# Optimization experiments

Hardware: AMD Instinct MI355X
Metric: run time of the kernel (lower is better)

Reference implementation:

```python
import jax, jax.numpy as jnp
import numpy as np

N = 100_000   # nodes
E = 1_600_000 # edges (avg degree 16)
IN = 128
OUT = 128
EPS = 1e-5    # torch BatchNorm1d default eps


def setup_inputs() -> dict:
    key = jax.random.key(0)
    k0, k1, k2 = jax.random.split(key, 3)
    x = jax.random.normal(k0, (N, IN), dtype=jnp.float32)
    edge_index = jax.random.randint(k1, (2, E), 0, N, dtype=jnp.int32)
    W = jax.random.normal(k2, (IN, OUT), dtype=jnp.float32) * (1.0 / np.sqrt(IN))
    b = jnp.zeros((OUT,), dtype=jnp.float32)
    gamma = jnp.ones((OUT,), dtype=jnp.float32)
    beta = jnp.zeros((OUT,), dtype=jnp.float32)
    return {"x": x, "edge_index": edge_index, "W": W, "b": b, "gamma": gamma, "beta": beta}


def reference(x, edge_index, W, b, gamma, beta):
    n = x.shape[0]
    # --- GCNConv: add self loops + symmetric normalization (PyG gcn_norm) ---
    loops = jnp.arange(n, dtype=edge_index.dtype)
    row = jnp.concatenate([edge_index[0], loops])  # sources  [E+N]
    col = jnp.concatenate([edge_index[1], loops])  # targets  [E+N]
    deg = jax.ops.segment_sum(jnp.ones_like(col, dtype=x.dtype), col, num_segments=n)
    dinv = jnp.where(deg > 0, jax.lax.rsqrt(deg), 0.0)
    norm = dinv[row] * dinv[col]                    # [E+N]
    # linear transform first, then gather-scale-scatter
    h = x @ W                                       # [N, OUT]
    msg = h[row] * norm[:, None]                    # [E+N, OUT]
    out = jax.ops.segment_sum(msg, col, num_segments=n) + b  # [N, OUT]
    # --- BatchNorm1d (training mode: batch stats, biased var) ---
    mean = jnp.mean(out, axis=0)
    var = jnp.mean(jnp.square(out - mean), axis=0)
    y = (out - mean) * jax.lax.rsqrt(var + EPS) * gamma + beta
    # --- ReLU ---
    return jnp.maximum(y, 0.0)
```

## Files before the change

### kernel.cpp

```cpp
#include <hip/hip_runtime.h>
#include <cstddef>

#define F 128
#define EPSV 1e-5f
#define NBMAX 1024
#define PAD 2560
#define CHUNK 8192
#define EPT 16

typedef short bf16x8 __attribute__((ext_vector_type(8)));
typedef float f32x4 __attribute__((ext_vector_type(4)));

__device__ inline unsigned short f2bf(float v) {
  unsigned u = __float_as_uint(v);
  return (unsigned short)((u + 0x7fffu + ((u >> 16) & 1u)) >> 16);
}
__device__ inline float bf_lo(unsigned u) { return __uint_as_float(u << 16); }
__device__ inline float bf_hi(unsigned u) { return __uint_as_float(u & 0xffff0000u); }

__global__ __launch_bounds__(256) void k_init(const float* __restrict__ Wm,
                                              unsigned short* __restrict__ wt,
                                              int* __restrict__ gcur,
                                              float* __restrict__ stats) {
  int idx = blockIdx.x * 256 + threadIdx.x;
  if (idx < F * F) {
    int k = idx >> 7, c = idx & 127;
    wt[c * F + k] = f2bf(Wm[idx]);
  }
  if (idx < NBMAX) gcur[idx] = idx * PAD;
  if (idx < 512) stats[idx] = 0.0f;
}

__global__ __launch_bounds__(512) void k_binfill(const int* __restrict__ row,
                                                 const int* __restrict__ col,
                                                 int* __restrict__ gcur,
                                                 unsigned* __restrict__ pairs, int e) {
  __shared__ unsigned staged[CHUNK];
  __shared__ unsigned short sbid[CHUNK];
  __shared__ int cnt[NBMAX];
  __shared__ int scan[NBMAX];
  int t = threadIdx.x;
  int base0 = blockIdx.x * CHUNK;
  int valid = e - base0; if (valid > CHUNK) valid = CHUNK;
#pragma unroll
  for (int j = 0; j < 2; ++j) cnt[t + j * 512] = 0;
  __syncthreads();
  unsigned myb[EPT];
  unsigned mysl[EPT];
#pragma unroll
  for (int k = 0; k < EPT; ++k) {
    int i = t + k * 512;
    if (i < valid) {
      int c = col[base0 + i];
      int b = c >> 7;
      int seq = atomicAdd(&cnt[b], 1);
      myb[k] = (unsigned)b;
      mysl[k] = ((unsigned)seq << 7) | (unsigned)(c & 127);
    }
  }
  __syncthreads();
#pragma unroll
  for (int j = 0; j < 2; ++j) scan[t + j * 512] = cnt[t + j * 512];
  __syncthreads();
  for (int off = 1; off < NBMAX; off <<= 1) {
    int v[2];
#pragma unroll
    for (int j = 0; j < 2; ++j) { int i = t + j * 512; v[j] = (i >= off) ? scan[i - off] : 0; }
    __syncthreads();
#pragma unroll
    for (int j = 0; j < 2; ++j) scan[t + j * 512] += v[j];
    __syncthreads();
  }
#pragma unroll
  for (int k = 0; k < EPT; ++k) {
    int i = t + k * 512;
    if (i < valid) {
      int b = (int)myb[k];
      int lpos = (scan[b] - cnt[b]) + (int)(mysl[k] >> 7);
      unsigned src = (unsigned)row[base0 + i];
      staged[lpos] = (src << 7) | (mysl[k] & 127u);
      sbid[lpos] = (unsigned short)b;
    }
  }
  __syncthreads();
#pragma unroll
  for (int j = 0; j < 2; ++j) {
    int b = t + j * 512;
    int c = cnt[b];
    if (c > 0) {
      int lbase = scan[b] - c;
      int gbase = atomicAdd(&gcur[b], c);
      cnt[b] = gbase - lbase;
    }
  }
  __syncthreads();
  for (int i = t; i < valid; i += 512) {
    pairs[cnt[sbid[i]] + i] = staged[i];
  }
}

__global__ __launch_bounds__(256) void k_sort2(const int* __restrict__ gcur,
                                               const unsigned* __restrict__ pairs,
                                               int* __restrict__ rowbeg,
                                               int* __restrict__ rowend,
                                               int* __restrict__ srcs,
                                               float* __restrict__ dinv, int n) {
  __shared__ int cnt[128];
  __shared__ int pre[128];
  __shared__ int cur[128];
  int bkt = blockIdx.x;
  int node0 = bkt << 7;
  int nodes = n - node0; if (nodes > 128) nodes = 128;
  int t = threadIdx.x;
  int ebeg = bkt * PAD, eend = gcur[bkt];
  if (t < 128) cnt[t] = 0;
  __syncthreads();
  for (int i = ebeg + t; i < eend; i += 256) atomicAdd(&cnt[pairs[i] & 127u], 1);
  __syncthreads();
  if (t < 128) pre[t] = cnt[t];
  __syncthreads();
  for (int off = 1; off < 128; off <<= 1) {
    int v = 0;
    if (t < 128 && t >= off) v = pre[t - off];
    __syncthreads();
    if (t < 128) pre[t] += v;
    __syncthreads();
  }
  if (t < nodes) {
    int base = ebeg + pre[t] - cnt[t];
    rowbeg[node0 + t] = base;
    rowend[node0 + t] = base + cnt[t];
    cur[t] = base;
    dinv[node0 + t] = rsqrtf((float)(1 + cnt[t]));
  }
  __syncthreads();
  for (int i = ebeg + t; i < eend; i += 256) {
    unsigned pk = pairs[i];
    int pos = atomicAdd(&cur[pk & 127u], 1);
    srcs[pos] = (int)(pk >> 7);
  }
}

__global__ __launch_bounds__(256) void k_gemm(const float* __restrict__ x,
                                              const unsigned short* __restrict__ wt,
                                              const float* __restrict__ dinv,
                                              unsigned short* __restrict__ hb, int n) {
  __shared__ unsigned short xs[64 * 136];
  int t = threadIdx.x;
  int row0 = blockIdx.x * 64;
  {
    int c4 = t & 31;
    int rr = t >> 5;
#pragma unroll
    for (int it = 0; it < 8; ++it) {
      int r = rr + it * 8;
      int gr = row0 + r;
      if (gr < n) {
        const f32x4* xp = (const f32x4*)&x[(size_t)gr * F + c4 * 4];
        f32x4 v = __builtin_nontemporal_load(xp);
        unsigned p0 = (unsigned)f2bf(v.x) | ((unsigned)f2bf(v.y) << 16);
        unsigned p1 = (unsigned)f2bf(v.z) | ((unsigned)f2bf(v.w) << 16);
        uint2 pv; pv.x = p0; pv.y = p1;
        *(uint2*)&xs[r * 136 + c4 * 4] = pv;
      }
    }
  }
  __syncthreads();

  int w = t >> 6, l = t & 63;
  int lo = l & 15, hi = l >> 4;
  bf16x8 a[4];
#pragma unroll
  for (int ks = 0; ks < 4; ++ks)
    a[ks] = *(const bf16x8*)&xs[(w * 16 + lo) * 136 + ks * 32 + hi * 8];

  f32x4 acc[8];
#pragma unroll
  for (int ct = 0; ct < 8; ++ct) acc[ct] = (f32x4){0.f, 0.f, 0.f, 0.f};

  const unsigned short* wb = wt + lo * F + hi * 8;
#pragma unroll
  for (int ct = 0; ct < 8; ++ct) {
#pragma unroll
    for (int ks = 0; ks < 4; ++ks) {
      bf16x8 bf = *(const bf16x8*)(wb + ct * 16 * F + ks * 32);
      acc[ct] = __builtin_amdgcn_mfma_f32_16x16x32_bf16(a[ks], bf, acc[ct], 0, 0, 0);
    }
  }

  int node_base = row0 + w * 16 + hi * 4;
  float dv[4];
#pragma unroll
  for (int rg = 0; rg < 4; ++rg) {
    int node = node_base + rg;
    dv[rg] = (node < n) ? dinv[node] : 0.f;
  }
#pragma unroll
  for (int ct = 0; ct < 8; ++ct) {
#pragma unroll
    for (int rg = 0; rg < 4; ++rg) {
      int node = node_base + rg;
      if (node < n) hb[(size_t)node * F + ct * 16 + lo] = f2bf(acc[ct][rg] * dv[rg]);
    }
  }
}

__global__ __launch_bounds__(256) void k_gather(const int* __restrict__ rowbeg,
                                                const int* __restrict__ rowend,
                                                const float* __restrict__ dinv,
                                                const unsigned* __restrict__ hb32,
                                                const int* __restrict__ srcs,
                                                const float* __restrict__ bias,
                                                unsigned* __restrict__ outb32, int n) {
  int node = blockIdx.x * 4 + (threadIdx.x >> 6);
  if (node >= n) return;
  int lane = threadIdx.x & 63;
  float dc = dinv[node];
  int beg = rowbeg[node], end = rowend[node];

  unsigned hw = hb32[(size_t)node * 64 + lane];
  float ax = bf_lo(hw);
  float ay = bf_hi(hw);

  for (int chunk = beg; chunk < end; chunk += 64) {
    int m = end - chunk; if (m > 64) m = 64;
    int myidx = 0;
    if (chunk + lane < end) myidx = __builtin_nontemporal_load(&srcs[chunk + lane]);
    int j = 0;
    for (; j + 8 <= m; j += 8) {
      int s0 = __shfl(myidx, j),     s1 = __shfl(myidx, j + 1);
      int s2 = __shfl(myidx, j + 2), s3 = __shfl(myidx, j + 3);
      int s4 = __shfl(myidx, j + 4), s5 = __shfl(myidx, j + 5);
      int s6 = __shfl(myidx, j + 6), s7 = __shfl(myidx, j + 7);
      unsigned a0 = hb32[(size_t)s0 * 64 + lane];
      unsigned a1 = hb32[(size_t)s1 * 64 + lane];
      unsigned a2 = hb32[(size_t)s2 * 64 + lane];
      unsigned a3 = hb32[(size_t)s3 * 64 + lane];
      unsigned a4 = hb32[(size_t)s4 * 64 + lane];
      unsigned a5 = hb32[(size_t)s5 * 64 + lane];
      unsigned a6 = hb32[(size_t)s6 * 64 + lane];
      unsigned a7 = hb32[(size_t)s7 * 64 + lane];
      ax += bf_lo(a0); ay += bf_hi(a0);
      ax += bf_lo(a1); ay += bf_hi(a1);
      ax += bf_lo(a2); ay += bf_hi(a2);
      ax += bf_lo(a3); ay += bf_hi(a3);
      ax += bf_lo(a4); ay += bf_hi(a4);
      ax += bf_lo(a5); ay += bf_hi(a5);
      ax += bf_lo(a6); ay += bf_hi(a6);
      ax += bf_lo(a7); ay += bf_hi(a7);
    }
    for (; j < m; ++j) {
      int s0 = __shfl(myidx, j);
      unsigned a0 = hb32[(size_t)s0 * 64 + lane];
      ax += bf_lo(a0); ay += bf_hi(a0);
    }
  }
  float2 bv = *(const float2*)&bias[lane * 2];
  unsigned pack = (unsigned)f2bf(bv.x + dc * ax) | ((unsigned)f2bf(bv.y + dc * ay) << 16);
  __builtin_nontemporal_store(pack, &outb32[(size_t)node * 64 + lane]);
}

__global__ __launch_bounds__(256) void k_stats(const unsigned* __restrict__ outb32,
                                               float* __restrict__ stats, int n) {
  int p = threadIdx.x & 63;
  int g = threadIdx.x >> 6;
  int rpb = (n + gridDim.x - 1) / gridDim.x;
  int r0 = blockIdx.x * rpb;
  int r1 = r0 + rpb; if (r1 > n) r1 = n;
  float s0 = 0.f, q0 = 0.f, s1 = 0.f, q1 = 0.f;
  for (int r = r0 + g; r < r1; r += 4) {
    unsigned u = outb32[(size_t)r * 64 + p];
    float v0 = bf_lo(u), v1 = bf_hi(u);
    s0 += v0; q0 += v0 * v0; s1 += v1; q1 += v1 * v1;
  }
  __shared__ float sh[4][64][4];
  sh[g][p][0] = s0; sh[g][p][1] = q0; sh[g][p][2] = s1; sh[g][p][3] = q1;
  __syncthreads();
  if (g == 0) {
    float a = 0.f, b = 0.f, c = 0.f, d = 0.f;
#pragma unroll
    for (int j = 0; j < 4; ++j) {
      a += sh[j][p][0]; b += sh[j][p][1]; c += sh[j][p][2]; d += sh[j][p][3];
    }
    atomicAdd(&stats[2 * p], a);     atomicAdd(&stats[F + 2 * p], b);
    atomicAdd(&stats[2 * p + 1], c); atomicAdd(&stats[F + 2 * p + 1], d);
  }
}

__global__ __launch_bounds__(256) void k_apply(const unsigned* __restrict__ outb32,
                                               float* __restrict__ out,
                                               const float* __restrict__ stats,
                                               const float* __restrict__ gamma,
                                               const float* __restrict__ beta, int n) {
  long long i = (long long)blockIdx.x * 256 + threadIdx.x;
  if (i >= (long long)n * 64) return;
  int p = (int)i & 63;
  float inv_n = 1.0f / (float)n;
  unsigned u = __builtin_nontemporal_load(&outb32[i]);
  float v0 = bf_lo(u), v1 = bf_hi(u);
  float m0 = stats[2 * p] * inv_n;
  float var0 = stats[F + 2 * p] * inv_n - m0 * m0;
  float sc0 = gamma[2 * p] * rsqrtf(var0 + EPSV);
  float sf0 = beta[2 * p] - m0 * sc0;
  float m1 = stats[2 * p + 1] * inv_n;
  float var1 = stats[F + 2 * p + 1] * inv_n - m1 * m1;
  float sc1 = gamma[2 * p + 1] * rsqrtf(var1 + EPSV);
  float sf1 = beta[2 * p + 1] - m1 * sc1;
  float2 o;
  o.x = fmaxf(v0 * sc0 + sf0, 0.f);
  o.y = fmaxf(v1 * sc1 + sf1, 0.f);
  *(float2*)&out[i * 2] = o;
}

extern "C" void kernel_launch(void* const* d_in, const int* in_sizes, int n_in,
                              void* d_out, int out_size, void* d_ws, size_t ws_size,
                              hipStream_t stream) {
  const float* x     = (const float*)d_in[0];
  const int*   ei    = (const int*)d_in[1];
  const float* W     = (const float*)d_in[2];
  const float* b     = (const float*)d_in[3];
  const float* gamma = (const float*)d_in[4];
  const float* beta  = (const float*)d_in[5];
  int n = in_sizes[0] / F;
  int e = in_sizes[1] / 2;
  const int* row = ei;
  const int* col = ei + e;

  float* out = (float*)d_out;
  int nb = (n + 127) >> 7;
  int nchunk = (e + CHUNK - 1) / CHUNK;

  char* wp = (char*)d_ws;
  unsigned short* hb = (unsigned short*)wp;            wp += (size_t)n * F * 2;
  unsigned* outb32   = (unsigned*)wp;                  wp += (size_t)n * 64 * 4;
  float* dinv        = (float*)wp;                     wp += (size_t)n * 4;
  float* stats       = (float*)wp;                     wp += 512 * 4;
  int* gcur          = (int*)wp;                       wp += NBMAX * 4;
  int* rowbeg        = (int*)wp;                       wp += (size_t)n * 4;
  int* rowend        = (int*)wp;                       wp += (size_t)n * 4;
  unsigned* pairs    = (unsigned*)wp;                  wp += (size_t)NBMAX * PAD * 4;
  int* srcs          = (int*)wp;                       wp += (size_t)NBMAX * PAD * 4;
  unsigned short* wt = (unsigned short*)wp;            wp += (size_t)F * F * 2;

  k_init   <<<(F * F + 255) / 256, 256, 0, stream>>>(W, wt, gcur, stats);
  k_binfill<<<nchunk, 512, 0, stream>>>(row, col, gcur, pairs, e);
  k_sort2  <<<nb, 256, 0, stream>>>(gcur, pairs, rowbeg, rowend, srcs, dinv, n);
  k_gemm   <<<(n + 63) / 64, 256, 0, stream>>>(x, wt, dinv, hb, n);
  k_gather <<<(n + 3) / 4, 256, 0, stream>>>(rowbeg, rowend, dinv, (const unsigned*)hb, srcs, b, outb32, n);
  k_stats  <<<512, 256, 0, stream>>>(outb32, stats, n);
  k_apply  <<<(int)(((long long)n * 64 + 255) / 256), 256, 0, stream>>>(outb32, out, stats, gamma, beta, n);
}
```

Measured before the change: 217.6 us.

## Fuse gather, BN stats and apply into one cooperative persistent kernel

Replaces the separate gather, stats and apply kernels with a single cooperative kernel using a grid-stride persistent loop. Column statistics are accumulated in registers from the freshly computed bf16 outputs, which removes the full re-read of outb32 that the stats kernel used to do. A grid-wide sync then separates the statistics from the normalize+ReLU pass. This also saves two launches. The cost is grid-sync overhead and a grid capped at 2048 blocks, which may give less latency hiding for the irregular gather than the original one-block-per-4-nodes launch.

```diff
diff --git a/kernel.cpp b/kernel.cpp
--- a/kernel.cpp
+++ b/kernel.cpp
@@ -1,4 +1,5 @@
 #include <hip/hip_runtime.h>
+#include <hip/hip_cooperative_groups.h>
 #include <cstddef>
 
 #define F 128
@@ -205,99 +206,90 @@
   }
 }
 
-__global__ __launch_bounds__(256) void k_gather(const int* __restrict__ rowbeg,
-                                                const int* __restrict__ rowend,
-                                                const float* __restrict__ dinv,
-                                                const unsigned* __restrict__ hb32,
-                                                const int* __restrict__ srcs,
-                                                const float* __restrict__ bias,
-                                                unsigned* __restrict__ outb32, int n) {
-  int node = blockIdx.x * 4 + (threadIdx.x >> 6);
-  if (node >= n) return;
-  int lane = threadIdx.x & 63;
-  float dc = dinv[node];
-  int beg = rowbeg[node], end = rowend[node];
-
-  unsigned hw = hb32[(size_t)node * 64 + lane];
-  float ax = bf_lo(hw);
-  float ay = bf_hi(hw);
-
-  for (int chunk = beg; chunk < end; chunk += 64) {
-    int m = end - chunk; if (m > 64) m = 64;
-    int myidx = 0;
-    if (chunk + lane < end) myidx = __builtin_nontemporal_load(&srcs[chunk + lane]);
-    int j = 0;
-    for (; j + 8 <= m; j += 8) {
-      int s0 = __shfl(myidx, j),     s1 = __shfl(myidx, j + 1);
-      int s2 = __shfl(myidx, j + 2), s3 = __shfl(myidx, j + 3);
-      int s4 = __shfl(myidx, j + 4), s5 = __shfl(myidx, j + 5);
-      int s6 = __shfl(myidx, j + 6), s7 = __shfl(myidx, j + 7);
-      unsigned a0 = hb32[(size_t)s0 * 64 + lane];
-      unsigned a1 = hb32[(size_t)s1 * 64 + lane];
-      unsigned a2 = hb32[(size_t)s2 * 64 + lane];
-      unsigned a3 = hb32[(size_t)s3 * 64 + lane];
-      unsigned a4 = hb32[(size_t)s4 * 64 + lane];
-      unsigned a5 = hb32[(size_t)s5 * 64 + lane];
-      unsigned a6 = hb32[(size_t)s6 * 64 + lane];
-      unsigned a7 = hb32[(size_t)s7 * 64 + lane];
-      ax += bf_lo(a0); ay += bf_hi(a0);
-      ax += bf_lo(a1); ay += bf_hi(a1);
-      ax += bf_lo(a2); ay += bf_hi(a2);
-      ax += bf_lo(a3); ay += bf_hi(a3);
-      ax += bf_lo(a4); ay += bf_hi(a4);
-      ax += bf_lo(a5); ay += bf_hi(a5);
-      ax += bf_lo(a6); ay += bf_hi(a6);
-      ax += bf_lo(a7); ay += bf_hi(a7);
-    }
-    for (; j < m; ++j) {
-      int s0 = __shfl(myidx, j);
-      unsigned a0 = hb32[(size_t)s0 * 64 + lane];
-      ax += bf_lo(a0); ay += bf_hi(a0);
-    }
-  }
-  float2 bv = *(const float2*)&bias[lane * 2];
-  unsigned pack = (unsigned)f2bf(bv.x + dc * ax) | ((unsigned)f2bf(bv.y + dc * ay) << 16);
-  __builtin_nontemporal_store(pack, &outb32[(size_t)node * 64 + lane]);
-}
-
-__global__ __launch_bounds__(256) void k_stats(const unsigned* __restrict__ outb32,
-                                               float* __restrict__ stats, int n) {
-  int p = threadIdx.x & 63;
-  int g = threadIdx.x >> 6;
-  int rpb = (n + gridDim.x - 1) / gridDim.x;
-  int r0 = blockIdx.x * rpb;
-  int r1 = r0 + rpb; if (r1 > n) r1 = n;
+__global__ __launch_bounds__(256, 8) void k_fused(const int* rowbeg,
+                                                  const int* rowend,
+                                                  const float* dinv,
+                                                  const unsigned* hb32,
+                                                  const int* srcs,
+                                                  const float* bias,
+                                                  unsigned* outb32,
+                                                  float* stats,
+                                                  const float* gamma,
+                                                  const float* beta,
+                                                  float* out, int n) {
+  cooperative_groups::grid_group grid = cooperative_groups::this_grid();
+  int t = threadIdx.x;
+  int w = t >> 6, lane = t & 63;
+  int ng = (n + 3) >> 2;
   float s0 = 0.f, q0 = 0.f, s1 = 0.f, q1 = 0.f;
-  for (int r = r0 + g; r < r1; r += 4) {
-    unsigned u = outb32[(size_t)r * 64 + p];
-    float v0 = bf_lo(u), v1 = bf_hi(u);
-    s0 += v0; q0 += v0 * v0; s1 += v1; q1 += v1 * v1;
-  }
+
+  for (int g = blockIdx.x; g < ng; g += gridDim.x) {
+    int node = g * 4 + w;
+    if (node < n) {
+      float dc = dinv[node];
+      int beg = rowbeg[node], end = rowend[node];
+      unsigned hw = hb32[(size_t)node * 64 + lane];
+      float ax = bf_lo(hw);
+      float ay = bf_hi(hw);
+      for (int chunk = beg; chunk < end; chunk += 64) {
+        int m = end - chunk; if (m > 64) m = 64;
+        int myidx = 0;
+        if (chunk + lane < end) myidx = __builtin_nontemporal_load(&srcs[chunk + lane]);
+        int j = 0;
+        for (; j + 8 <= m; j += 8) {
+          int v0 = __shfl(myidx, j),     v1 = __shfl(myidx, j + 1);
+          int v2 = __shfl(myidx, j + 2), v3 = __shfl(myidx, j + 3);
+          int v4 = __shfl(myidx, j + 4), v5 = __shfl(myidx, j + 5);
+          int v6 = __shfl(myidx, j + 6), v7 = __shfl(myidx, j + 7);
+          unsigned a0 = hb32[(size_t)v0 * 64 + lane];
+          unsigned a1 = hb32[(size_t)v1 * 64 + lane];
+          unsigned a2 = hb32[(size_t)v2 * 64 + lane];
+          unsigned a3 = hb32[(size_t)v3 * 64 + lane];
+          unsigned a4 = hb32[(size_t)v4 * 64 + lane];
+          unsigned a5 = hb32[(size_t)v5 * 64 + lane];
+          unsigned a6 = hb32[(size_t)v6 * 64 + lane];
+          unsigned a7 = hb32[(size_t)v7 * 64 + lane];
+          ax += bf_lo(a0); ay += bf_hi(a0);
+          ax += bf_lo(a1); ay += bf_hi(a1);
+          ax += bf_lo(a2); ay += bf_hi(a2);
+          ax += bf_lo(a3); ay += bf_hi(a3);
+          ax += bf_lo(a4); ay += bf_hi(a4);
+          ax += bf_lo(a5); ay += bf_hi(a5);
+          ax += bf_lo(a6); ay += bf_hi(a6);
+          ax += bf_lo(a7); ay += bf_hi(a7);
+        }
+        for (; j < m; ++j) {
+          int sj = __shfl(myidx, j);
+          unsigned a0 = hb32[(size_t)sj * 64 + lane];
+          ax += bf_lo(a0); ay += bf_hi(a0);
+        }
+      }
+      float2 bv = *(const float2*)&bias[lane * 2];
+      unsigned pack = (unsigned)f2bf(bv.x + dc * ax) |
+                      ((unsigned)f2bf(bv.y + dc * ay) << 16);
+      __builtin_nontemporal_store(pack, &outb32[(size_t)node * 64 + lane]);
+      float r0 = bf_lo(pack), r1 = bf_hi(pack);
+      s0 += r0; q0 += r0 * r0; s1 += r1; q1 += r1 * r1;
+    }
+  }
+
   __shared__ float sh[4][64][4];
-  sh[g][p][0] = s0; sh[g][p][1] = q0; sh[g][p][2] = s1; sh[g][p][3] = q1;
-  __syncthreads();
-  if (g == 0) {
+  sh[w][lane][0] = s0; sh[w][lane][1] = q0; sh[w][lane][2] = s1; sh[w][lane][3] = q1;
+  __syncthreads();
+  if (w == 0) {
     float a = 0.f, b = 0.f, c = 0.f, d = 0.f;
 #pragma unroll
     for (int j = 0; j < 4; ++j) {
-      a += sh[j][p][0]; b += sh[j][p][1]; c += sh[j][p][2]; d += sh[j][p][3];
-    }
-    atomicAdd(&stats[2 * p], a);     atomicAdd(&stats[F + 2 * p], b);
-    atomicAdd(&stats[2 * p + 1], c); atomicAdd(&stats[F + 2 * p + 1], d);
-  }
-}
-
-__global__ __launch_bounds__(256) void k_apply(const unsigned* __restrict__ outb32,
-                                               float* __restrict__ out,
-                                               const float* __restrict__ stats,
-                                               const float* __restrict__ gamma,
-                                               const float* __restrict__ beta, int n) {
-  long long i = (long long)blockIdx.x * 256 + threadIdx.x;
-  if (i >= (long long)n * 64) return;
-  int p = (int)i & 63;
+      a += sh[j][lane][0]; b += sh[j][lane][1]; c += sh[j][lane][2]; d += sh[j][lane][3];
+    }
+    atomicAdd(&stats[2 * lane], a);     atomicAdd(&stats[F + 2 * lane], b);
+    atomicAdd(&stats[2 * lane + 1], c); atomicAdd(&stats[F + 2 * lane + 1], d);
+  }
+
+  grid.sync();
+
+  int p = t & 63;
   float inv_n = 1.0f / (float)n;
-  unsigned u = __builtin_nontemporal_load(&outb32[i]);
-  float v0 = bf_lo(u), v1 = bf_hi(u);
   float m0 = stats[2 * p] * inv_n;
   float var0 = stats[F + 2 * p] * inv_n - m0 * m0;
   float sc0 = gamma[2 * p] * rsqrtf(var0 + EPSV);
@@ -306,10 +298,15 @@
   float var1 = stats[F + 2 * p + 1] * inv_n - m1 * m1;
   float sc1 = gamma[2 * p + 1] * rsqrtf(var1 + EPSV);
   float sf1 = beta[2 * p + 1] - m1 * sc1;
-  float2 o;
-  o.x = fmaxf(v0 * sc0 + sf0, 0.f);
-  o.y = fmaxf(v1 * sc1 + sf1, 0.f);
-  *(float2*)&out[i * 2] = o;
+  long long tot = (long long)n * 64;
+  long long stride = (long long)gridDim.x * 256;
+  for (long long i = (long long)blockIdx.x * 256 + t; i < tot; i += stride) {
+    unsigned u = __builtin_nontemporal_load(&outb32[i]);
+    float2 o;
+    o.x = fmaxf(bf_lo(u) * sc0 + sf0, 0.f);
+    o.y = fmaxf(bf_hi(u) * sc1 + sf1, 0.f);
+    *(float2*)&out[i * 2] = o;
+  }
 }
 
 extern "C" void kernel_launch(void* const* d_in, const int* in_sizes, int n_in,
@@ -346,7 +343,16 @@
   k_binfill<<<nchunk, 512, 0, stream>>>(row, col, gcur, pairs, e);
   k_sort2  <<<nb, 256, 0, stream>>>(gcur, pairs, rowbeg, rowend, srcs, dinv, n);
   k_gemm   <<<(n + 63) / 64, 256, 0, stream>>>(x, wt, dinv, hb, n);
-  k_gather <<<(n + 3) / 4, 256, 0, stream>>>(rowbeg, rowend, dinv, (const unsigned*)hb, srcs, b, outb32, n);
-  k_stats  <<<512, 256, 0, stream>>>(outb32, stats, n);
-  k_apply  <<<(int)(((long long)n * 64 + 255) / 256), 256, 0, stream>>>(outb32, out, stats, gamma, beta, n);
-}
+
+  int maxb = 0;
+  (void)hipOccupancyMaxActiveBlocksPerMultiprocessor(&maxb, k_fused, 256, 0);
+  if (maxb < 1) maxb = 1;
+  int grid = maxb * 256;
+  if (grid > 2048) grid = 2048;
+  const unsigned* hb32c = (const unsigned*)hb;
+  void* args[] = {(void*)&rowbeg, (void*)&rowend, (void*)&dinv, (void*)&hb32c,
+                  (void*)&srcs, (void*)&b, (void*)&outb32, (void*)&stats,
+                  (void*)&gamma, (void*)&beta, (void*)&out, (void*)&n};
+  (void)hipLaunchCooperativeKernel((void*)k_fused, dim3(grid), dim3(256),
+                                   args, 0, stream);
+}
```

Result: slower. 367.1 us (+68.7%).
